# Kernel tuning notes

Measured on AMD Instinct MI355X. Metric: run time of the kernel, lower is better.

## Reference

```python
import jax, jax.numpy as jnp
import numpy as np

H = 16  # n_heads


def _ln(x, g, b, eps=1e-5):
    m = x.mean(-1, keepdims=True)
    v = ((x - m) ** 2).mean(-1, keepdims=True)
    return (x - m) / jnp.sqrt(v + eps) * g + b


def setup_inputs() -> dict:
    key = jax.random.key(0)
    ks = jax.random.split(key, 10)
    b, lq, d, dff, L = 2, 1024, 1024, 4096, 4
    s = 0.02
    return {
        "x": jax.random.normal(ks[0], (b, lq, d), jnp.float32),
        "memory_bank": jax.random.normal(ks[1], (L, b, lq, d), jnp.float32),
        "attn_mask": jax.random.bernoulli(ks[2], 0.3, (b, lq, lq)),
        "ln1_g": jnp.ones((d,), jnp.float32),
        "ln1_b": jnp.zeros((d,), jnp.float32),
        "Wq": jax.random.normal(ks[3], (d, d), jnp.float32) * s,
        "Wk": jax.random.normal(ks[4], (d, d), jnp.float32) * s,
        "Wv": jax.random.normal(ks[5], (d, d), jnp.float32) * s,
        "Wo": jax.random.normal(ks[6], (d, d), jnp.float32) * s,
        "ln2_g": jnp.ones((d,), jnp.float32),
        "ln2_b": jnp.zeros((d,), jnp.float32),
        "W1": jax.random.normal(ks[7], (d, dff), jnp.float32) * s,
        "b1": jnp.zeros((dff,), jnp.float32),
        "W2": jax.random.normal(ks[8], (dff, d), jnp.float32) * s,
        "b2": jnp.zeros((d,), jnp.float32),
    }


def reference(x, memory_bank, attn_mask, ln1_g, ln1_b, Wq, Wk, Wv, Wo,
              ln2_g, ln2_b, W1, b1, W2, b2):
    # x: [b, lq, d]; memory_bank: [L, b, lk, d]; attn_mask: [b, lq, lk] bool (True = masked)
    b, lq, d = x.shape
    dh = d // H
    # preprocess_attn: LayerNorm (eval mode -> dropouts are identity)
    q = _ln(x, ln1_g, ln1_b)
    # grow memory bank with current normalized input
    mem = jnp.concatenate([memory_bank, q[None]], axis=0)  # [L+1, b, lk, d]
    L, _, lk, _ = mem.shape
    # projections (bias-free); key/value projected per layer then flattened over (L, lk)
    pq = (q @ Wq).reshape(b, lq, H, dh).transpose(0, 2, 1, 3) * (dh ** -0.5)  # [b,h,lq,dh]
    pk = (mem @ Wk).transpose(1, 0, 2, 3).reshape(b, L * lk, H, dh).transpose(0, 2, 1, 3)
    pv = (mem @ Wv).transpose(1, 0, 2, 3).reshape(b, L * lk, H, dh).transpose(0, 2, 1, 3)
    scores = jnp.einsum('bhqd,bhkd->bhqk', pq, pk)           # [b,h,lq,L*lk]
    scores = scores.reshape(b, H, lq, L, lk)
    scores = jnp.where(attn_mask[:, None, :, None, :], -jnp.inf, scores)
    attn = jax.nn.softmax(scores.reshape(b, H, lq, L * lk), axis=-1)
    ctx = jnp.einsum('bhqk,bhkd->bhqd', attn, pv)            # [b,h,lq,dh]
    ctx = ctx.transpose(0, 2, 1, 3).reshape(b, lq, d)
    attn_out = ctx @ Wo
    # postprocess_attn: residual add
    x2 = x + attn_out
    # FFN: LayerNorm -> Linear -> ReLU -> Linear -> residual
    f = _ln(x2, ln2_g, ln2_b)
    f = jax.nn.relu(f @ W1 + b1) @ W2 + b2
    out = x2 + f
    return (out, mem)
```

## Files before the change

### kernel.cpp

```cpp
#include <hip/hip_runtime.h>
#include <hip/hip_bf16.h>

typedef __attribute__((ext_vector_type(8))) __bf16 bf16x8;
typedef __attribute__((ext_vector_type(4))) __bf16 bf16x4;
typedef __attribute__((ext_vector_type(4))) float f32x4;
typedef __attribute__((ext_vector_type(16))) float f32x16;

#define MFMA16(a, b, c) __builtin_amdgcn_mfma_f32_16x16x32_bf16((a), (b), (c), 0, 0, 0)
#define MFMA32(a, b, c) __builtin_amdgcn_mfma_f32_32x32x16_bf16((a), (b), (c), 0, 0, 0)
#define LOG2E 1.4426950408889634f

static __device__ __forceinline__ float exp2_fast(float x) {
    float r; asm("v_exp_f32 %0, %1" : "=v"(r) : "v"(x)); return r;
}

__device__ __forceinline__ void gll16(const void* g, void* l) {
    __builtin_amdgcn_global_load_lds((const __attribute__((address_space(1))) void*)g,
                                     (__attribute__((address_space(3))) void*)l,
                                     16, 0, 0);
}

__global__ __launch_bounds__(256) void prep_kernel(const float* __restrict__ bank,
                                                   float* __restrict__ mem_out,
                                                   __bf16* __restrict__ membf,
                                                   const float* __restrict__ x,
                                                   const float* __restrict__ g,
                                                   const float* __restrict__ bta,
                                                   float* __restrict__ q_out,
                                                   __bf16* __restrict__ qbf,
                                                   const float* __restrict__ Wq,
                                                   const float* __restrict__ Wk,
                                                   const float* __restrict__ Wv,
                                                   __bf16* __restrict__ Wq_t,
                                                   __bf16* __restrict__ Wkv_t) {
    __shared__ float rs[4], rs2[4];
    __shared__ float tile[32][33];
    int blk = blockIdx.x;
    if (blk < 2048) {
        int i = blk * 256 + threadIdx.x;
        const float4* i4 = (const float4*)bank;
        float4* o4 = (float4*)mem_out;
        for (; i < 2097152; i += 2048 * 256) {
            float4 v = i4[i];
            o4[i] = v;
            if (membf) {
                bf16x4 ob = {(__bf16)v.x, (__bf16)v.y, (__bf16)v.z, (__bf16)v.w};
                ((bf16x4*)membf)[i] = ob;
            }
        }
    } else if (blk < 4096) {
        int row = blk - 2048;
        const float4 v = ((const float4*)(x + (size_t)row * 1024))[threadIdx.x];
        float s = v.x + v.y + v.z + v.w;
        float s2 = v.x * v.x + v.y * v.y + v.z * v.z + v.w * v.w;
#pragma unroll
        for (int off = 1; off < 64; off <<= 1) {
            s += __shfl_xor(s, off);
            s2 += __shfl_xor(s2, off);
        }
        int wv = threadIdx.x >> 6;
        if ((threadIdx.x & 63) == 0) { rs[wv] = s; rs2[wv] = s2; }
        __syncthreads();
        s = rs[0] + rs[1] + rs[2] + rs[3];
        s2 = rs2[0] + rs2[1] + rs2[2] + rs2[3];
        float mean = s * (1.0f / 1024.0f);
        float var = s2 * (1.0f / 1024.0f) - mean * mean;
        float rstd = rsqrtf(var + 1e-5f);
        float4 gg = ((const float4*)g)[threadIdx.x];
        float4 bb = ((const float4*)bta)[threadIdx.x];
        float4 o;
        o.x = (v.x - mean) * rstd * gg.x + bb.x;
        o.y = (v.y - mean) * rstd * gg.y + bb.y;
        o.z = (v.z - mean) * rstd * gg.z + bb.z;
        o.w = (v.w - mean) * rstd * gg.w + bb.w;
        ((float4*)(q_out + (size_t)row * 1024))[threadIdx.x] = o;
        if (qbf) {
            bf16x4 ob = {(__bf16)o.x, (__bf16)o.y, (__bf16)o.z, (__bf16)o.w};
            ((bf16x4*)(qbf + (size_t)row * 1024))[threadIdx.x] = ob;
        }
    } else {
        int w = blk - 4096;
        int sel = w >> 10, within = w & 1023;
        const float* in = (sel == 0) ? Wq : ((sel == 1) ? Wk : Wv);
        __bf16* out = (sel == 0) ? Wq_t : (Wkv_t + (size_t)(sel - 1) * 1048576);
        int k0 = (within >> 5) * 32, n0 = (within & 31) * 32;
        int tx = threadIdx.x & 31, ty = threadIdx.x >> 5;
#pragma unroll
        for (int i = 0; i < 4; i++)
            tile[ty + i * 8][tx] = in[(size_t)(k0 + ty + i * 8) * 1024 + n0 + tx];
        __syncthreads();
#pragma unroll
        for (int i = 0; i < 4; i++)
            out[(size_t)(n0 + ty + i * 8) * 1024 + k0 + tx] = (__bf16)tile[tx][ty + i * 8];
    }
}

__global__ __launch_bounds__(256) void vtr_kernel(const __bf16* __restrict__ PV,
                                                  __bf16* __restrict__ PVt,
                                                  const unsigned char* __restrict__ mask,
                                                  unsigned int* __restrict__ mbits) {
    __shared__ __bf16 tile[64][72];
    int w = blockIdx.x;
    if (w < 2560) {
        int bh = w / 80, kt = w % 80;
        int b = bh >> 4, h = bh & 15;
        int lidx = kt >> 4, i0 = (kt & 15) * 64;
        int kg0 = lidx * 2048 + b * 1024 + i0;
        int r = threadIdx.x >> 2, c16 = (threadIdx.x & 3) * 16;
        const __bf16* src = PV + (size_t)(kg0 + r) * 1024 + h * 64 + c16;
        *(bf16x8*)&tile[r][c16] = *(const bf16x8*)src;
        *(bf16x8*)&tile[r][c16 + 8] = *(const bf16x8*)(src + 8);
        __syncthreads();
        int dh = threadIdx.x >> 2, k0 = (threadIdx.x & 3) * 16;
        bf16x8 o0, o1;
#pragma unroll
        for (int j = 0; j < 8; j++) {
            o0[j] = tile[k0 + j][dh];
            o1[j] = tile[k0 + 8 + j][dh];
        }
        __bf16* dst = PVt + (size_t)(bh * 64 + dh) * 5120 + kt * 64 + k0;
        *(bf16x8*)dst = o0;
        *(bf16x8*)(dst + 8) = o1;
    } else {
        int row = w - 2560;
        const unsigned char* mrow = mask + (size_t)row * 1024;
        int wv = threadIdx.x >> 6, l = threadIdx.x & 63;
        unsigned long long* dst = (unsigned long long*)(mbits + (size_t)row * 32);
#pragma unroll
        for (int i = 0; i < 4; i++) {
            int key = i * 256 + wv * 64 + l;
            unsigned long long bal = __ballot(mrow[key] != 0);
            if (l == 0) dst[i * 4 + wv] = bal;
        }
    }
}

__global__ __launch_bounds__(256) void ln_kernel(const float* __restrict__ x,
                                                 const float* __restrict__ g,
                                                 const float* __restrict__ bta,
                                                 __bf16* __restrict__ outb) {
    int row = blockIdx.x;
    const float4 v = ((const float4*)(x + (size_t)row * 1024))[threadIdx.x];
    float s = v.x + v.y + v.z + v.w;
    float s2 = v.x * v.x + v.y * v.y + v.z * v.z + v.w * v.w;
#pragma unroll
    for (int off = 1; off < 64; off <<= 1) {
        s += __shfl_xor(s, off);
        s2 += __shfl_xor(s2, off);
    }
    __shared__ float rs[4], rs2[4];
    int wv = threadIdx.x >> 6;
    if ((threadIdx.x & 63) == 0) { rs[wv] = s; rs2[wv] = s2; }
    __syncthreads();
    s = rs[0] + rs[1] + rs[2] + rs[3];
    s2 = rs2[0] + rs2[1] + rs2[2] + rs2[3];
    float mean = s * (1.0f / 1024.0f);
    float var = s2 * (1.0f / 1024.0f) - mean * mean;
    float rstd = rsqrtf(var + 1e-5f);
    float4 gg = ((const float4*)g)[threadIdx.x];
    float4 bb = ((const float4*)bta)[threadIdx.x];
    bf16x4 ob;
    ob[0] = (__bf16)((v.x - mean) * rstd * gg.x + bb.x);
    ob[1] = (__bf16)((v.y - mean) * rstd * gg.y + bb.y);
    ob[2] = (__bf16)((v.z - mean) * rstd * gg.z + bb.z);
    ob[3] = (__bf16)((v.w - mean) * rstd * gg.w + bb.w);
    ((bf16x4*)(outb + (size_t)row * 1024))[threadIdx.x] = ob;
}

__global__ __launch_bounds__(256) void comb_ln2(const float* __restrict__ pc0,
                                                const float* __restrict__ pc1,
                                                const float* __restrict__ x,
                                                const float* __restrict__ g,
                                                const float* __restrict__ bta,
                                                float* __restrict__ x2,
                                                __bf16* __restrict__ fln) {
    int row = blockIdx.x;
    int idx = row * 256 + threadIdx.x;
    float4 a = ((const float4*)pc0)[idx];
    float4 b = ((const float4*)pc1)[idx];
    float4 r = ((const float4*)x)[idx];
    float4 v;
    v.x = a.x + b.x + r.x;
    v.y = a.y + b.y + r.y;
    v.z = a.z + b.z + r.z;
    v.w = a.w + b.w + r.w;
    ((float4*)x2)[idx] = v;
    float s = v.x + v.y + v.z + v.w;
    float s2 = v.x * v.x + v.y * v.y + v.z * v.z + v.w * v.w;
#pragma unroll
    for (int off = 1; off < 64; off <<= 1) {
        s += __shfl_xor(s, off);
        s2 += __shfl_xor(s2, off);
    }
    __shared__ float rs[4], rs2[4];
    int wv = threadIdx.x >> 6;
    if ((threadIdx.x & 63) == 0) { rs[wv] = s; rs2[wv] = s2; }
    __syncthreads();
    s = rs[0] + rs[1] + rs[2] + rs[3];
    s2 = rs2[0] + rs2[1] + rs2[2] + rs2[3];
    float mean = s * (1.0f / 1024.0f);
    float var = s2 * (1.0f / 1024.0f) - mean * mean;
    float rstd = rsqrtf(var + 1e-5f);
    float4 gg = ((const float4*)g)[threadIdx.x];
    float4 bb = ((const float4*)bta)[threadIdx.x];
    bf16x4 ob;
    ob[0] = (__bf16)((v.x - mean) * rstd * gg.x + bb.x);
    ob[1] = (__bf16)((v.y - mean) * rstd * gg.y + bb.y);
    ob[2] = (__bf16)((v.z - mean) * rstd * gg.z + bb.z);
    ob[3] = (__bf16)((v.w - mean) * rstd * gg.w + bb.w);
    ((bf16x4*)(fln + (size_t)row * 1024))[threadIdx.x] = ob;
}

__device__ __forceinline__ void tr_body(const float* __restrict__ in, __bf16* __restrict__ out,
                                        int K, int N, int k0, int n0) {
    __shared__ float tile[32][33];
    int tx = threadIdx.x & 31, ty = threadIdx.x >> 5;
#pragma unroll
    for (int i = 0; i < 4; i++)
        tile[ty + i * 8][tx] = in[(size_t)(k0 + ty + i * 8) * N + n0 + tx];
    __syncthreads();
#pragma unroll
    for (int i = 0; i < 4; i++)
        out[(size_t)(n0 + ty + i * 8) * K + k0 + tx] = (__bf16)tile[tx][ty + i * 8];
}

__global__ __launch_bounds__(256) void tr_late(const float* __restrict__ Wo,
                                               const float* __restrict__ W1,
                                               const float* __restrict__ W2,
                                               __bf16* __restrict__ Wo_t,
                                               __bf16* __restrict__ W1_t,
                                               __bf16* __restrict__ W2_t) {
    int w = blockIdx.x;
    const float* in;
    __bf16* out;
    int K, N, k0, n0;
    if (w < 1024) {
        in = Wo; out = Wo_t; K = 1024; N = 1024; n0 = (w & 31) * 32; k0 = (w >> 5) * 32;
    } else if (w < 5120) {
        int v = w - 1024;
        in = W1; out = W1_t; K = 1024; N = 4096; n0 = (v & 127) * 32; k0 = (v >> 7) * 32;
    } else {
        int v = w - 5120;
        in = W2; out = W2_t; K = 4096; N = 1024; n0 = (v & 31) * 32; k0 = (v >> 5) * 32;
    }
    tr_body(in, out, K, N, k0, n0);
}

template <int EPI, bool ABF16>
__device__ __forceinline__ void gemm_core(const void* __restrict__ Av,
                                          const __bf16* __restrict__ Bt,
                                          void* __restrict__ Cout,
                                          const float* __restrict__ bias,
                                          const float* __restrict__ res,
                                          int N, int lda, int ldb, int klen,
                                          float scale, int bm, int bn) {
    constexpr int LDA = ABF16 ? 32 : 40;
    __shared__ __bf16 As[128 * LDA];
    __shared__ __bf16 Bs[128 * 32];

    int t = threadIdx.x;
    int lane = t & 63, wave = t >> 6;
    int wm = (wave >> 1) * 64, wn = (wave & 1) * 64;
    int l16 = lane & 15, l4 = lane >> 4;

    f32x4 acc[4][4];
#pragma unroll
    for (int m = 0; m < 4; m++)
#pragma unroll
        for (int n = 0; n < 4; n++) acc[m][n] = (f32x4){0.f, 0.f, 0.f, 0.f};

    int srow = t >> 2;
    int scol = (t & 3) * 8;
    int ar = t >> 1, ak = (t & 1) * 16;
    const __bf16* Ab = (const __bf16*)Av;
    const float* Af = (const float*)Av;

    for (int k0 = 0; k0 < klen; k0 += 32) {
        gll16(Bt + (size_t)(bn + srow) * ldb + (k0 + scol), &Bs[wave * 512]);
        gll16(Bt + (size_t)(bn + 64 + srow) * ldb + (k0 + scol), &Bs[2048 + wave * 512]);
        if constexpr (ABF16) {
            gll16(Ab + (size_t)(bm + srow) * lda + (k0 + scol), &As[wave * 512]);
            gll16(Ab + (size_t)(bm + 64 + srow) * lda + (k0 + scol), &As[2048 + wave * 512]);
        } else {
            const float* ap = Af + (size_t)(bm + ar) * lda + k0 + ak;
            float4 f0 = ((const float4*)ap)[0];
            float4 f1 = ((const float4*)ap)[1];
            float4 f2 = ((const float4*)ap)[2];
            float4 f3 = ((const float4*)ap)[3];
            float ta[16] = {f0.x, f0.y, f0.z, f0.w, f1.x, f1.y, f1.z, f1.w,
                            f2.x, f2.y, f2.z, f2.w, f3.x, f3.y, f3.z, f3.w};
            bf16x8 v0, v1;
#pragma unroll
            for (int j = 0; j < 8; j++) { v0[j] = (__bf16)ta[j]; v1[j] = (__bf16)ta[j + 8]; }
            *(bf16x8*)&As[ar * 40 + ak] = v0;
            *(bf16x8*)&As[ar * 40 + ak + 8] = v1;
        }
        __syncthreads();

        bf16x8 af[4], bfr[4];
#pragma unroll
        for (int m = 0; m < 4; m++) af[m] = *(const bf16x8*)&As[(wm + m * 16 + l16) * LDA + l4 * 8];
#pragma unroll
        for (int n = 0; n < 4; n++) bfr[n] = *(const bf16x8*)&Bs[(wn + n * 16 + l16) * 32 + l4 * 8];
#pragma unroll
        for (int m = 0; m < 4; m++)
#pragma unroll
            for (int n = 0; n < 4; n++) acc[m][n] = MFMA16(af[m], bfr[n], acc[m][n]);
        __syncthreads();
    }

#pragma unroll
    for (int m = 0; m < 4; m++) {
#pragma unroll
        for (int r = 0; r < 4; r++) {
            int row = bm + wm + m * 16 + l4 * 4 + r;
#pragma unroll
            for (int n = 0; n < 4; n++) {
                int col = bn + wn + n * 16 + l16;
                float c = acc[m][n][r];
                size_t idx = (size_t)row * N + col;
                if (EPI == 0) {
                    ((__bf16*)Cout)[idx] = (__bf16)(c * scale);
                } else if (EPI == 1) {
                    ((float*)Cout)[idx] = c + res[idx];
                } else if (EPI == 2) {
                    ((__bf16*)Cout)[idx] = (__bf16)fmaxf(c + bias[col], 0.0f);
                } else if (EPI == 3) {
                    ((float*)Cout)[idx] = c + bias[col] + res[idx];
                } else {
                    ((float*)Cout)[idx] = c;
                }
            }
        }
    }
}

template <int EPI, bool ABF16>
__global__ __launch_bounds__(256) void gemm_bt(const void* __restrict__ Av,
                                               const __bf16* __restrict__ Bt,
                                               void* __restrict__ Cout,
                                               const float* __restrict__ bias,
                                               const float* __restrict__ res,
                                               int N, int K, float scale, int nbx) {
    int q = gridDim.x >> 3;
    int swz = (blockIdx.x & 7) * q + (blockIdx.x >> 3);
    int bn = (swz % nbx) * 128;
    int bm = (swz / nbx) * 128;
    gemm_core<EPI, ABF16>(Av, Bt, Cout, bias, res, N, K, K, K, scale, bm, bn);
}

template <bool ABF16>
__global__ __launch_bounds__(256) void gemm_proj(const void* __restrict__ Akv,
                                                 const __bf16* __restrict__ Wkv_t,
                                                 __bf16* __restrict__ PK,
                                                 __bf16* __restrict__ PV,
                                                 const void* __restrict__ Aq,
                                                 const __bf16* __restrict__ Wq_t,
                                                 __bf16* __restrict__ Pq) {
    int q = gridDim.x >> 3;
    int swz = (blockIdx.x & 7) * q + (blockIdx.x >> 3);
    if (swz < 1280) {
        int bn = (swz & 15) * 128, bm = (swz >> 4) * 128;
        __bf16* C = (bn < 1024) ? PK : PV;
        int bnl = bn & 1023;
        const __bf16* Bt = Wkv_t + ((size_t)(bn & 1024) << 10);
        gemm_core<0, ABF16>(Akv, Bt, C, nullptr, nullptr, 1024, 1024, 1024, 1024, 1.0f, bm, bnl);
    } else {
        int p = swz - 1280;
        int bn = (p & 7) * 128, bm = (p >> 3) * 128;
        gemm_core<0, ABF16>(Aq, Wq_t, Pq, nullptr, nullptr, 1024, 1024, 1024, 1024,
                            0.125f * LOG2E, bm, bn);
    }
}

__global__ __launch_bounds__(256) void gemm_w2(const __bf16* __restrict__ h1,
                                               const __bf16* __restrict__ W2_t,
                                               float* __restrict__ pc0,
                                               float* __restrict__ pc1) {
    int q = gridDim.x >> 3;
    int swz = (blockIdx.x & 7) * q + (blockIdx.x >> 3);
    int half = swz >> 7;
    int p = swz & 127;
    int bn = (p & 7) * 128, bm = (p >> 3) * 128;
    int koff = half * 2048;
    gemm_core<4, true>(h1 + koff, W2_t + koff, half ? pc1 : pc0, nullptr, nullptr,
                       1024, 4096, 4096, 2048, 1.0f, bm, bn);
}

__global__ __launch_bounds__(256) void gemm_wo(const __bf16* __restrict__ ctx,
                                               const __bf16* __restrict__ Wo_t,
                                               float* __restrict__ pc0,
                                               float* __restrict__ pc1) {
    int q = gridDim.x >> 3;
    int swz = (blockIdx.x & 7) * q + (blockIdx.x >> 3);
    int half = swz >> 7;
    int p = swz & 127;
    int bn = (p & 7) * 128, bm = (p >> 3) * 128;
    int koff = half * 512;
    gemm_core<4, true>(ctx + koff, Wo_t + koff, half ? pc1 : pc0, nullptr, nullptr,
                       1024, 1024, 1024, 512, 1.0f, bm, bn);
}

__global__ __launch_bounds__(256) void comb_kernel(const float* __restrict__ pc0,
                                                   const float* __restrict__ pc1,
                                                   const float* __restrict__ bias,
                                                   const float* __restrict__ res,
                                                   float* __restrict__ out) {
    int i = blockIdx.x * 256 + threadIdx.x;
    float4 a = ((const float4*)pc0)[i];
    float4 b = ((const float4*)pc1)[i];
    float4 r = ((const float4*)res)[i];
    float4 o;
    o.x = a.x + b.x + r.x;
    o.y = a.y + b.y + r.y;
    o.z = a.z + b.z + r.z;
    o.w = a.w + b.w + r.w;
    if (bias) {
        float4 bb = ((const float4*)bias)[i & 255];
        o.x += bb.x; o.y += bb.y; o.z += bb.z; o.w += bb.w;
    }
    ((float4*)out)[i] = o;
}

__device__ __forceinline__ void softmax_p(const f32x16& s0, const f32x16& s1,
                                          unsigned int mka, unsigned int mkb,
                                          int hi, float& lsum, bf16x8* pf) {
    unsigned int ow[8][2];
#pragma unroll
    for (int g = 0; g < 4; g++) {
        bf16x4 p0, p1;
#pragma unroll
        for (int m = 0; m < 4; m++) {
            float e = exp2_fast(s0[g * 4 + m]);
            e = ((mka >> (g * 8 + hi * 4 + m)) & 1u) ? 0.0f : e;
            lsum += e;
            p0[m] = (__bf16)e;
            float e2 = exp2_fast(s1[g * 4 + m]);
            e2 = ((mkb >> (g * 8 + hi * 4 + m)) & 1u) ? 0.0f : e2;
            lsum += e2;
            p1[m] = (__bf16)e2;
        }
        ow[g][0] = ((unsigned int*)&p0)[0];
        ow[g][1] = ((unsigned int*)&p0)[1];
        ow[4 + g][0] = ((unsigned int*)&p1)[0];
        ow[4 + g][1] = ((unsigned int*)&p1)[1];
    }
#pragma unroll
    for (int ks = 0; ks < 4; ks++) {
        unsigned int a0 = ow[2 * ks][0], b0 = ow[2 * ks + 1][0];
        unsigned int a1 = ow[2 * ks][1], b1 = ow[2 * ks + 1][1];
        asm volatile("v_permlane32_swap_b32 %0, %1" : "+v"(a0), "+v"(b0));
        asm volatile("v_permlane32_swap_b32 %0, %1" : "+v"(a1), "+v"(b1));
        unsigned int* pp = (unsigned int*)&pf[ks];
        pp[0] = a0; pp[1] = a1; pp[2] = b0; pp[3] = b1;
    }
}

#define NCHP 20
__global__ __launch_bounds__(256, 2) void attn_part(const __bf16* __restrict__ Pq,
                                                    const __bf16* __restrict__ PK,
                                                    const __bf16* __restrict__ PVt,
                                                    const unsigned int* __restrict__ mbits,
                                                    __bf16* __restrict__ pacc,
                                                    float* __restrict__ pl) {
    int bh = blockIdx.x;
    int b = bh >> 4, h = bh & 15;
    int rng = blockIdx.z;
    int wave = threadIdx.x >> 6, lane = threadIdx.x & 63;
    int l32 = lane & 31, hi = lane >> 5;
    int q0 = blockIdx.y * 256 + wave * 64;

    __shared__ __bf16 KB[2][64][64];
    __shared__ __bf16 VB[2][64][64];

    bf16x8 qf[2][4];
#pragma unroll
    for (int tile = 0; tile < 2; tile++) {
        const __bf16* pqrow = Pq + (size_t)(b * 1024 + q0 + tile * 32 + l32) * 1024 + h * 64 + hi * 8;
#pragma unroll
        for (int ds = 0; ds < 4; ds++) qf[tile][ds] = *(const bf16x8*)(pqrow + ds * 16);
    }

    f32x16 acc00, acc01, acc10, acc11;
#pragma unroll
    for (int i = 0; i < 16; i++) { acc00[i] = 0.f; acc01[i] = 0.f; acc10[i] = 0.f; acc11[i] = 0.f; }
    float lsum0 = 0.0f, lsum1 = 0.0f;

    const unsigned int* mrow0 = mbits + (size_t)(b * 1024 + q0 + l32) * 32;
    const unsigned int* mrow1 = mbits + (size_t)(b * 1024 + q0 + 32 + l32) * 32;

    int kgbase = rng * 1280;

    int idxA = wave * 8 + (lane >> 3);
    int idxB = (wave + 4) * 8 + (lane >> 3);
    int GA = (idxA ^ (idxA >> 3)) & 7;
    int GB = (idxB ^ (idxB >> 3)) & 7;
    int swA = (((lane & 7) ^ GA) << 4);
    int swB = (((lane & 7) ^ GB) << 4);
    size_t koffA = (size_t)idxA * 2048 + swA;
    size_t koffB = (size_t)idxB * 2048 + swB;
    size_t voffA = (size_t)idxA * 10240 + swA;
    size_t voffB = (size_t)idxB * 10240 + swB;

    int kmod = kgbase & 1023;
    const char* pkc = (const char*)PK + ((size_t)((kgbase >> 10) * 2048 + b * 1024 + kmod)) * 2048
                      + (size_t)h * 128;
    const char* pvc = (const char*)PVt + (size_t)(bh * 64) * 10240 + (size_t)kgbase * 2;

#define STAGE(BUF)                                            \
    do {                                                      \
        gll16(pkc + koffA, &KB[BUF][wave * 8][0]);            \
        gll16(pkc + koffB, &KB[BUF][(wave + 4) * 8][0]);      \
        gll16(pvc + voffA, &VB[BUF][wave * 8][0]);            \
        gll16(pvc + voffB, &VB[BUF][(wave + 4) * 8][0]);      \
    } while (0)
#define ADV()                                                          \
    do {                                                               \
        int st = (kmod + 64 >= 1024) ? (64 + 1024) : 64;               \
        kmod = (kmod + 64) & 1023;                                     \
        pkc += (size_t)st * 2048;                                      \
        pvc += 128;                                                    \
    } while (0)

    STAGE(0);
    ADV();
    int kd0 = (kgbase & 1023) >> 5;
    unsigned int mk0a = mrow0[kd0], mk0b = mrow0[kd0 + 1];
    unsigned int mk1a = mrow1[kd0], mk1b = mrow1[kd0 + 1];

    int Gr0 = (l32 ^ (l32 >> 3)) & 7;
    int r1v = 32 + l32;
    int Gr1 = (r1v ^ (r1v >> 3)) & 7;

    for (int t = 0; t < NCHP; t++) {
        int buf = t & 1;
        __syncthreads();
        if (t + 1 < NCHP) {
            STAGE(buf ^ 1);
            ADV();
        }
        unsigned int nk0a = 0, nk0b = 0, nk1a = 0, nk1b = 0;
        if (t + 1 < NCHP) {
            int kdn = ((kgbase + (t + 1) * 64) & 1023) >> 5;
            nk0a = mrow0[kdn]; nk0b = mrow0[kdn + 1];
            nk1a = mrow1[kdn]; nk1b = mrow1[kdn + 1];
        }

        const __bf16* KsF = &KB[buf][0][0];
        const __bf16* VtF = &VB[buf][0][0];

        f32x16 s00, s01, s10, s11;
#pragma unroll
        for (int i = 0; i < 16; i++) { s00[i] = 0.f; s01[i] = 0.f; s10[i] = 0.f; s11[i] = 0.f; }
        __builtin_amdgcn_s_setprio(1);
#pragma unroll
        for (int ds = 0; ds < 4; ds++) {
            bf16x8 ka0 = *(const bf16x8*)&KsF[l32 * 64 + (((ds * 2 + hi) ^ Gr0) << 3)];
            bf16x8 ka1 = *(const bf16x8*)&KsF[r1v * 64 + (((ds * 2 + hi) ^ Gr1) << 3)];
            s00 = MFMA32(ka0, qf[0][ds], s00);
            s10 = MFMA32(ka0, qf[1][ds], s10);
            s01 = MFMA32(ka1, qf[0][ds], s01);
            s11 = MFMA32(ka1, qf[1][ds], s11);
        }
        __builtin_amdgcn_s_setprio(0);

        bf16x8 pf0[4], pf1[4];
        softmax_p(s00, s01, mk0a, mk0b, hi, lsum0, pf0);
        softmax_p(s10, s11, mk1a, mk1b, hi, lsum1, pf1);

        mk0a = nk0a; mk0b = nk0b; mk1a = nk1a; mk1b = nk1b;

        __builtin_amdgcn_s_setprio(1);
#pragma unroll
        for (int ks = 0; ks < 4; ks++) {
            bf16x8 vf0 = *(const bf16x8*)&VtF[l32 * 64 + (((ks * 2 + hi) ^ Gr0) << 3)];
            bf16x8 vf1 = *(const bf16x8*)&VtF[r1v * 64 + (((ks * 2 + hi) ^ Gr1) << 3)];
            acc00 = MFMA32(vf0, pf0[ks], acc00);
            acc01 = MFMA32(vf1, pf0[ks], acc01);
            acc10 = MFMA32(vf0, pf1[ks], acc10);
            acc11 = MFMA32(vf1, pf1[ks], acc11);
        }
        __builtin_amdgcn_s_setprio(0);
    }
#undef STAGE
#undef ADV

    lsum0 += __shfl_xor(lsum0, 32);
    lsum1 += __shfl_xor(lsum1, 32);

    size_t blk = ((size_t)(bh * 4 + blockIdx.y) * 4 + rng);
    __bf16* pa0 = pacc + blk * 16384 + (size_t)(wave * 64 + l32) * 64;
    __bf16* pa1 = pacc + blk * 16384 + (size_t)(wave * 64 + 32 + l32) * 64;
#pragma unroll
    for (int g = 0; g < 4; g++) {
        bf16x4 o00, o01, o10, o11;
#pragma unroll
        for (int m = 0; m < 4; m++) {
            o00[m] = (__bf16)acc00[g * 4 + m];
            o01[m] = (__bf16)acc01[g * 4 + m];
            o10[m] = (__bf16)acc10[g * 4 + m];
            o11[m] = (__bf16)acc11[g * 4 + m];
        }
        *(bf16x4*)&pa0[g * 8 + hi * 4] = o00;
        *(bf16x4*)&pa0[32 + g * 8 + hi * 4] = o01;
        *(bf16x4*)&pa1[g * 8 + hi * 4] = o10;
        *(bf16x4*)&pa1[32 + g * 8 + hi * 4] = o11;
    }
    if (hi == 0) {
        pl[blk * 256 + wave * 64 + l32] = lsum0;
        pl[blk * 256 + wave * 64 + 32 + l32] = lsum1;
    }
}

__global__ __launch_bounds__(512) void attn_comb(const __bf16* __restrict__ pacc,
                                                 const float* __restrict__ pl,
                                                 __bf16* __restrict__ ctx) {
    int bh = blockIdx.x, qb = blockIdx.y;
    int b = bh >> 4, h = bh & 15;
    int q = threadIdx.x >> 1, dhalf = (threadIdx.x & 1) * 32;
    float acc[32];
#pragma unroll
    for (int j = 0; j < 32; j++) acc[j] = 0.0f;
    float l = 0.0f;
    size_t blk0 = ((size_t)(bh * 4 + qb)) * 4;
#pragma unroll
    for (int rng = 0; rng < 4; rng++) {
        size_t base = (blk0 + rng) * 16384 + (size_t)q * 64 + dhalf;
#pragma unroll
        for (int v = 0; v < 4; v++) {
            bf16x8 a = *(const bf16x8*)&pacc[base + v * 8];
#pragma unroll
            for (int j = 0; j < 8; j++) acc[v * 8 + j] += (float)a[j];
        }
        l += pl[(blk0 + rng) * 256 + q];
    }
    float inv = 1.0f / l;
    __bf16* crow = ctx + ((size_t)(b * 1024 + qb * 256 + q) << 10) + h * 64 + dhalf;
#pragma unroll
    for (int v = 0; v < 4; v++) {
        bf16x8 o;
#pragma unroll
        for (int j = 0; j < 8; j++) o[j] = (__bf16)(acc[v * 8 + j] * inv);
        *(bf16x8*)&crow[v * 8] = o;
    }
}

#define KHALF 2560
#define CK 64
#define NCH 40
__global__ __launch_bounds__(512, 4) void attn_kernel(const __bf16* __restrict__ Pq,
                                                      const __bf16* __restrict__ PK,
                                                      const __bf16* __restrict__ PV,
                                                      const unsigned char* __restrict__ mask,
                                                      __bf16* __restrict__ ctx) {
    int bh = blockIdx.x;
    int b = bh >> 4, h = bh & 15;
    int wave = threadIdx.x >> 6, lane = threadIdx.x & 63;
    int grp = wave >> 2, wv = wave & 3;
    int l16 = lane & 15, l4 = lane >> 4;
    int q0 = blockIdx.y * 64 + wv * 16;

    __shared__ __bf16 Ks[2][64][72];
    __shared__ __bf16 Vt[2][64][72];
    __shared__ __bf16 Ps[8][16][72];

    const f32x4 fzero = {0.f, 0.f, 0.f, 0.f};

    bf16x8 qf[2];
    {
        const __bf16* pqrow = Pq + (size_t)(b * 1024 + q0 + l16) * 1024 + h * 64;
        qf[0] = *(const bf16x8*)(pqrow + l4 * 8);
        qf[1] = *(const bf16x8*)(pqrow + 32 + l4 * 8);
    }

    f32x4 accT[4];
#pragma unroll
    for (int n = 0; n < 4; n++) accT[n] = fzero;
    float lsum = 0.0f;

    const unsigned char* mrow_p = mask + (size_t)b * (1024u * 1024u) + (size_t)(q0 + l16) * 1024;

    int tl = threadIdx.x & 255;
    int skey = tl >> 2;
    int sd0 = (tl & 3) << 4;
    int kgbase = grp * KHALF;

    bf16x8 rk0, rk1, rv0, rv1;
    unsigned int mk[4], mkn[4];
    {
        int kg = kgbase + skey;
        int lidx = kg >> 10, i = kg & 1023;
        size_t off = (size_t)(lidx * 2048 + b * 1024 + i) * 1024 + h * 64 + sd0;
        rk0 = *(const bf16x8*)(PK + off);
        rk1 = *(const bf16x8*)(PK + off + 8);
        rv0 = *(const bf16x8*)(PV + off);
        rv1 = *(const bf16x8*)(PV + off + 8);
        int kloc = kgbase & 1023;
#pragma unroll
        for (int tile = 0; tile < 4; tile++)
            mk[tile] = *(const unsigned int*)(mrow_p + kloc + tile * 16 + l4 * 4);
    }

    for (int t = 0; t < NCH; t++) {
        *(bf16x8*)&Ks[grp][skey][sd0] = rk0;
        *(bf16x8*)&Ks[grp][skey][sd0 + 8] = rk1;
#pragma unroll
        for (int j = 0; j < 8; j++) {
            int row = sd0 + j;
            Vt[grp][row][skey ^ ((row >> 3) << 3)] = rv0[j];
            int row2 = sd0 + 8 + j;
            Vt[grp][row2][skey ^ ((row2 >> 3) << 3)] = rv1[j];
        }
        __syncthreads();

        if (t + 1 < NCH) {
            int kg = kgbase + (t + 1) * CK + skey;
            int lidx = kg >> 10, i = kg & 1023;
            size_t off = (size_t)(lidx * 2048 + b * 1024 + i) * 1024 + h * 64 + sd0;
            rk0 = *(const bf16x8*)(PK + off);
            rk1 = *(const bf16x8*)(PK + off + 8);
            rv0 = *(const bf16x8*)(PV + off);
            rv1 = *(const bf16x8*)(PV + off + 8);
            int kloc = (kgbase + (t + 1) * CK) & 1023;
#pragma unroll
            for (int tile = 0; tile < 4; tile++)
                mkn[tile] = *(const unsigned int*)(mrow_p + kloc + tile * 16 + l4 * 4);
        }

        f32x4 s[4];
        __builtin_amdgcn_s_setprio(1);
#pragma unroll
        for (int tile = 0; tile < 4; tile++) {
            bf16x8 ka = *(const bf16x8*)&Ks[grp][tile * 16 + l16][l4 * 8];
            bf16x8 kb = *(const bf16x8*)&Ks[grp][tile * 16 + l16][32 + l4 * 8];
            f32x4 sz = fzero;
            sz = MFMA16(ka, qf[0], sz);
            sz = MFMA16(kb, qf[1], sz);
            s[tile] = sz;
        }
        __builtin_amdgcn_s_setprio(0);

        float psum = 0.0f;
#pragma unroll
        for (int tile = 0; tile < 4; tile++) {
            bf16x4 pk_;
#pragma unroll
            for (int r = 0; r < 4; r++) {
                float e = exp2_fast(s[tile][r]);
                e = ((mk[tile] >> (r * 8)) & 255u) ? 0.0f : e;
                psum += e;
                pk_[r] = (__bf16)e;
            }
            *(bf16x4*)&Ps[wave][l16][tile * 16 + l4 * 4] = pk_;
        }
        lsum += psum;
#pragma unroll
        for (int tile = 0; tile < 4; tile++) mk[tile] = mkn[tile];

        __builtin_amdgcn_s_setprio(1);
#pragma unroll
        for (int kk = 0; kk < 2; kk++) {
            bf16x8 pf = *(const bf16x8*)&Ps[wave][l16][kk * 32 + l4 * 8];
#pragma unroll
            for (int n = 0; n < 4; n++) {
                int row = n * 16 + l16;
                int colblk = (kk * 32 + l4 * 8) ^ ((row >> 3) << 3);
                bf16x8 vf = *(const bf16x8*)&Vt[grp][row][colblk];
                accT[n] = MFMA16(vf, pf, accT[n]);
            }
        }
        __builtin_amdgcn_s_setprio(0);
        __syncthreads();
    }

    lsum += __shfl_xor(lsum, 16);
    lsum += __shfl_xor(lsum, 32);

    float* exAcc = (float*)&Ks[0][0][0];
    float* exL = (float*)&Vt[0][0][0];
    if (grp == 1) {
#pragma unroll
        for (int n = 0; n < 4; n++)
            *(f32x4*)&exAcc[(wv * 16 + l16) * 68 + n * 16 + l4 * 4] = accT[n];
        if (l4 == 0) exL[wv * 16 + l16] = lsum;
    }
    __syncthreads();
    if (grp == 0) {
        int qi = wv * 16 + l16;
        float inv = 1.0f / (lsum + exL[qi]);
        __bf16* crow = ctx + ((size_t)(b * 1024 + q0 + l16) << 10) + h * 64;
#pragma unroll
        for (int n = 0; n < 4; n++) {
            f32x4 a1 = *(const f32x4*)&exAcc[qi * 68 + n * 16 + l4 * 4];
            bf16x4 o;
#pragma unroll
            for (int r = 0; r < 4; r++) o[r] = (__bf16)((accT[n][r] + a1[r]) * inv);
            *(bf16x4*)&crow[n * 16 + l4 * 4] = o;
        }
    }
}

extern "C" void kernel_launch(void* const* d_in, const int* in_sizes, int n_in,
                              void* d_out, int out_size, void* d_ws, size_t ws_size,
                              hipStream_t stream) {
    const float* x = (const float*)d_in[0];
    const float* memory_bank = (const float*)d_in[1];
    const unsigned char* attn_mask = (const unsigned char*)d_in[2];
    const float* ln1_g = (const float*)d_in[3];
    const float* ln1_b = (const float*)d_in[4];
    const float* Wq = (const float*)d_in[5];
    const float* Wk = (const float*)d_in[6];
    const float* Wv = (const float*)d_in[7];
    const float* Wo = (const float*)d_in[8];
    const float* ln2_g = (const float*)d_in[9];
    const float* ln2_b = (const float*)d_in[10];
    const float* W1 = (const float*)d_in[11];
    const float* b1 = (const float*)d_in[12];
    const float* W2 = (const float*)d_in[13];
    const float* b2 = (const float*)d_in[14];

    float* out = (float*)d_out;
    float* mem_out = out + 2097152;
    float* q_out = mem_out + 4 * 2097152;

    char* ws = (char*)d_ws;
    bool big = ws_size >= (70ull << 20);

    __bf16* PK = (__bf16*)ws;
    __bf16* PV = (__bf16*)(ws + (20ull << 20));
    __bf16 *Pq, *Wq_t, *Wkv_t, *ctx, *membf = nullptr, *qbf = nullptr;
    __bf16* PVt = nullptr;
    __bf16* pacc = nullptr;
    float* plv = nullptr;
    unsigned int* mbits = nullptr;
    if (big) {
        membf = (__bf16*)(ws + (40ull << 20));
        qbf = membf + (size_t)8192 * 1024;
        Wq_t = (__bf16*)(ws + (60ull << 20));
        Wkv_t = (__bf16*)(ws + (62ull << 20));
        Pq = (__bf16*)(ws + (66ull << 20));
        PVt = (__bf16*)(ws + (40ull << 20));
        mbits = (unsigned int*)(ws + (60ull << 20));
        pacc = (__bf16*)(ws + (20ull << 20));
        plv = (float*)(ws + (36ull << 20));
        ctx = (__bf16*)(ws + (60ull << 20));
    } else {
        Pq = (__bf16*)(ws + (40ull << 20));
        Wq_t = (__bf16*)(ws + (44ull << 20));
        Wkv_t = (__bf16*)(ws + (46ull << 20));
        ctx = (__bf16*)(ws + (44ull << 20));
    }
    __bf16* Wo_t = (__bf16*)ws;
    __bf16* W1_t = (__bf16*)(ws + (2ull << 20));
    __bf16* W2_t = (__bf16*)(ws + (10ull << 20));
    float* x2 = (float*)(ws + (18ull << 20));
    __bf16* fln = (__bf16*)(ws + (26ull << 20));
    __bf16* h1 = (__bf16*)(ws + (30ull << 20));
    float* wo_pc0 = (float*)(ws + (30ull << 20));
    float* wo_pc1 = (float*)(ws + (38ull << 20));
    float* pc0 = (float*)(ws + (46ull << 20));
    float* pc1 = (float*)(ws + (54ull << 20));

    prep_kernel<<<7168, 256, 0, stream>>>(memory_bank, mem_out, membf, x, ln1_g, ln1_b,
                                          q_out, qbf, Wq, Wk, Wv, Wq_t, Wkv_t);

    if (big)
        gemm_proj<true><<<1408, 256, 0, stream>>>(membf, Wkv_t, PK, PV, qbf, Wq_t, Pq);
    else
        gemm_proj<false><<<1408, 256, 0, stream>>>(mem_out, Wkv_t, PK, PV, q_out, Wq_t, Pq);

    if (big) {
        vtr_kernel<<<4608, 256, 0, stream>>>(PV, PVt, attn_mask, mbits);
        attn_part<<<dim3(32, 4, 4), 256, 0, stream>>>(Pq, PK, PVt, mbits, pacc, plv);
        attn_comb<<<dim3(32, 4), 512, 0, stream>>>(pacc, plv, ctx);
    } else {
        attn_kernel<<<dim3(32, 16), 512, 0, stream>>>(Pq, PK, PV, attn_mask, ctx);
    }

    tr_late<<<9216, 256, 0, stream>>>(Wo, W1, W2, Wo_t, W1_t, W2_t);

    if (big) {
        gemm_wo<<<256, 256, 0, stream>>>(ctx, Wo_t, wo_pc0, wo_pc1);
        comb_ln2<<<2048, 256, 0, stream>>>(wo_pc0, wo_pc1, x, ln2_g, ln2_b, x2, fln);
    } else {
        gemm_bt<1, true><<<128, 256, 0, stream>>>(ctx, Wo_t, x2, nullptr, x, 1024, 1024, 1.0f, 8);
        ln_kernel<<<2048, 256, 0, stream>>>(x2, ln2_g, ln2_b, fln);
    }
    gemm_bt<2, true><<<512, 256, 0, stream>>>(fln, W1_t, h1, b1, nullptr, 4096, 1024, 1.0f, 32);
    if (big) {
        gemm_w2<<<256, 256, 0, stream>>>(h1, W2_t, pc0, pc1);
        comb_kernel<<<2048, 256, 0, stream>>>(pc0, pc1, b2, x2, out);
    } else {
        gemm_bt<3, true><<<128, 256, 0, stream>>>(h1, W2_t, out, b2, x2, 1024, 4096, 1.0f, 8);
    }
}
```

Measured before the change: 272.9 us.

## Add K=64 bf16 GEMM core with direct-to-LDS loads and 8-way attention split

Adds a new bf16 GEMM core that stages 128x64 A/B tiles via global_load_lds with an XOR swizzle and runs 16x16x32 MFMAs. It is used for the QKV projection, Wo, W1 and W2 GEMMs on the large-workspace path. The attention partial kernel is templated on the number of key ranges, and 8 ranges are used when the workspace is at least 104 MB, giving more blocks for occupancy. The cost is more partial output for the combine step. The new GEMM core is single-buffered with two barriers per K step, so load latency may not be hidden as well as in the old core.

```diff
diff --git a/kernel.cpp b/kernel.cpp
--- a/kernel.cpp
+++ b/kernel.cpp
@@ -335,6 +335,100 @@
     }
 }
 
+template <int EPI>
+__device__ __forceinline__ void gemm_core64(const __bf16* __restrict__ Ab,
+                                            const __bf16* __restrict__ Bt,
+                                            void* __restrict__ Cout,
+                                            const float* __restrict__ bias,
+                                            const float* __restrict__ res,
+                                            int N, int lda, int ldb, int klen,
+                                            float scale, int bm, int bn) {
+    __shared__ __bf16 As[128 * 64];
+    __shared__ __bf16 Bs[128 * 64];
+
+    int t = threadIdx.x;
+    int lane = t & 63, wave = t >> 6;
+    int wm = (wave >> 1) * 64, wn = (wave & 1) * 64;
+    int l16 = lane & 15, l4 = lane >> 4;
+
+    f32x4 acc[4][4];
+#pragma unroll
+    for (int m = 0; m < 4; m++)
+#pragma unroll
+        for (int n = 0; n < 4; n++) acc[m][n] = (f32x4){0.f, 0.f, 0.f, 0.f};
+
+    int lrow = lane >> 3, lg = lane & 7;
+    size_t srcA[4], srcB[4];
+    __bf16 *dstA[4], *dstB[4];
+#pragma unroll
+    for (int c = 0; c < 4; c++) {
+        int grow = c * 32 + wave * 8 + lrow;
+        int G = (grow ^ (grow >> 3)) & 7;
+        srcA[c] = (size_t)(bm + grow) * lda + ((lg ^ G) << 3);
+        srcB[c] = (size_t)(bn + grow) * ldb + ((lg ^ G) << 3);
+        dstA[c] = &As[(c * 32 + wave * 8) * 64];
+        dstB[c] = &Bs[(c * 32 + wave * 8) * 64];
+    }
+    int GA[4], GB[4];
+#pragma unroll
+    for (int m = 0; m < 4; m++) {
+        int ra = wm + m * 16 + l16;
+        GA[m] = (ra ^ (ra >> 3)) & 7;
+        int rb = wn + m * 16 + l16;
+        GB[m] = (rb ^ (rb >> 3)) & 7;
+    }
+
+    for (int k0 = 0; k0 < klen; k0 += 64) {
+#pragma unroll
+        for (int c = 0; c < 4; c++) {
+            gll16(Ab + srcA[c] + k0, dstA[c]);
+            gll16(Bt + srcB[c] + k0, dstB[c]);
+        }
+        __syncthreads();
+#pragma unroll
+        for (int kh = 0; kh < 2; kh++) {
+            bf16x8 af[4], bfr[4];
+#pragma unroll
+            for (int m = 0; m < 4; m++) {
+                int ga = (kh * 4 + l4) ^ GA[m];
+                af[m] = *(const bf16x8*)&As[(wm + m * 16 + l16) * 64 + ga * 8];
+                int gb = (kh * 4 + l4) ^ GB[m];
+                bfr[m] = *(const bf16x8*)&Bs[(wn + m * 16 + l16) * 64 + gb * 8];
+            }
+#pragma unroll
+            for (int m = 0; m < 4; m++)
+#pragma unroll
+                for (int n = 0; n < 4; n++) acc[m][n] = MFMA16(af[m], bfr[n], acc[m][n]);
+        }
+        __syncthreads();
+    }
+
+#pragma unroll
+    for (int m = 0; m < 4; m++) {
+#pragma unroll
+        for (int r = 0; r < 4; r++) {
+            int row = bm + wm + m * 16 + l4 * 4 + r;
+#pragma unroll
+            for (int n = 0; n < 4; n++) {
+                int col = bn + wn + n * 16 + l16;
+                float c = acc[m][n][r];
+                size_t idx = (size_t)row * N + col;
+                if (EPI == 0) {
+                    ((__bf16*)Cout)[idx] = (__bf16)(c * scale);
+                } else if (EPI == 1) {
+                    ((float*)Cout)[idx] = c + res[idx];
+                } else if (EPI == 2) {
+                    ((__bf16*)Cout)[idx] = (__bf16)fmaxf(c + bias[col], 0.0f);
+                } else if (EPI == 3) {
+                    ((float*)Cout)[idx] = c + bias[col] + res[idx];
+                } else {
+                    ((float*)Cout)[idx] = c;
+                }
+            }
+        }
+    }
+}
+
 template <int EPI, bool ABF16>
 __global__ __launch_bounds__(256) void gemm_bt(const void* __restrict__ Av,
                                                const __bf16* __restrict__ Bt,
@@ -349,14 +443,27 @@
     gemm_core<EPI, ABF16>(Av, Bt, Cout, bias, res, N, K, K, K, scale, bm, bn);
 }
 
-template <bool ABF16>
-__global__ __launch_bounds__(256) void gemm_proj(const void* __restrict__ Akv,
-                                                 const __bf16* __restrict__ Wkv_t,
-                                                 __bf16* __restrict__ PK,
-                                                 __bf16* __restrict__ PV,
-                                                 const void* __restrict__ Aq,
-                                                 const __bf16* __restrict__ Wq_t,
-                                                 __bf16* __restrict__ Pq) {
+template <int EPI>
+__global__ __launch_bounds__(256) void gemm_bt64(const __bf16* __restrict__ Ab,
+                                                 const __bf16* __restrict__ Bt,
+                                                 void* __restrict__ Cout,
+                                                 const float* __restrict__ bias,
+                                                 const float* __restrict__ res,
+                                                 int N, int K, float scale, int nbx) {
+    int q = gridDim.x >> 3;
+    int swz = (blockIdx.x & 7) * q + (blockIdx.x >> 3);
+    int bn = (swz % nbx) * 128;
+    int bm = (swz / nbx) * 128;
+    gemm_core64<EPI>(Ab, Bt, Cout, bias, res, N, K, K, K, scale, bm, bn);
+}
+
+__global__ __launch_bounds__(256) void gemm_proj64(const __bf16* __restrict__ Akv,
+                                                   const __bf16* __restrict__ Wkv_t,
+                                                   __bf16* __restrict__ PK,
+                                                   __bf16* __restrict__ PV,
+                                                   const __bf16* __restrict__ Aq,
+                                                   const __bf16* __restrict__ Wq_t,
+                                                   __bf16* __restrict__ Pq) {
     int q = gridDim.x >> 3;
     int swz = (blockIdx.x & 7) * q + (blockIdx.x >> 3);
     if (swz < 1280) {
@@ -364,11 +471,34 @@
         __bf16* C = (bn < 1024) ? PK : PV;
         int bnl = bn & 1023;
         const __bf16* Bt = Wkv_t + ((size_t)(bn & 1024) << 10);
-        gemm_core<0, ABF16>(Akv, Bt, C, nullptr, nullptr, 1024, 1024, 1024, 1024, 1.0f, bm, bnl);
+        gemm_core64<0>(Akv, Bt, C, nullptr, nullptr, 1024, 1024, 1024, 1024, 1.0f, bm, bnl);
     } else {
         int p = swz - 1280;
         int bn = (p & 7) * 128, bm = (p >> 3) * 128;
-        gemm_core<0, ABF16>(Aq, Wq_t, Pq, nullptr, nullptr, 1024, 1024, 1024, 1024,
+        gemm_core64<0>(Aq, Wq_t, Pq, nullptr, nullptr, 1024, 1024, 1024, 1024,
+                       0.125f * LOG2E, bm, bn);
+    }
+}
+
+__global__ __launch_bounds__(256) void gemm_proj_f32(const void* __restrict__ Akv,
+                                                     const __bf16* __restrict__ Wkv_t,
+                                                     __bf16* __restrict__ PK,
+                                                     __bf16* __restrict__ PV,
+                                                     const void* __restrict__ Aq,
+                                                     const __bf16* __restrict__ Wq_t,
+                                                     __bf16* __restrict__ Pq) {
+    int q = gridDim.x >> 3;
+    int swz = (blockIdx.x & 7) * q + (blockIdx.x >> 3);
+    if (swz < 1280) {
+        int bn = (swz & 15) * 128, bm = (swz >> 4) * 128;
+        __bf16* C = (bn < 1024) ? PK : PV;
+        int bnl = bn & 1023;
+        const __bf16* Bt = Wkv_t + ((size_t)(bn & 1024) << 10);
+        gemm_core<0, false>(Akv, Bt, C, nullptr, nullptr, 1024, 1024, 1024, 1024, 1.0f, bm, bnl);
+    } else {
+        int p = swz - 1280;
+        int bn = (p & 7) * 128, bm = (p >> 3) * 128;
+        gemm_core<0, false>(Aq, Wq_t, Pq, nullptr, nullptr, 1024, 1024, 1024, 1024,
                             0.125f * LOG2E, bm, bn);
     }
 }
@@ -383,8 +513,8 @@
     int p = swz & 127;
     int bn = (p & 7) * 128, bm = (p >> 3) * 128;
     int koff = half * 2048;
-    gemm_core<4, true>(h1 + koff, W2_t + koff, half ? pc1 : pc0, nullptr, nullptr,
-                       1024, 4096, 4096, 2048, 1.0f, bm, bn);
+    gemm_core64<4>(h1 + koff, W2_t + koff, half ? pc1 : pc0, nullptr, nullptr,
+                   1024, 4096, 4096, 2048, 1.0f, bm, bn);
 }
 
 __global__ __launch_bounds__(256) void gemm_wo(const __bf16* __restrict__ ctx,
@@ -397,8 +527,8 @@
     int p = swz & 127;
     int bn = (p & 7) * 128, bm = (p >> 3) * 128;
     int koff = half * 512;
-    gemm_core<4, true>(ctx + koff, Wo_t + koff, half ? pc1 : pc0, nullptr, nullptr,
-                       1024, 1024, 1024, 512, 1.0f, bm, bn);
+    gemm_core64<4>(ctx + koff, Wo_t + koff, half ? pc1 : pc0, nullptr, nullptr,
+                   1024, 1024, 1024, 512, 1.0f, bm, bn);
 }
 
 __global__ __launch_bounds__(256) void comb_kernel(const float* __restrict__ pc0,
@@ -456,13 +586,14 @@
     }
 }
 
-#define NCHP 20
+template <int NRNG>
 __global__ __launch_bounds__(256, 2) void attn_part(const __bf16* __restrict__ Pq,
                                                     const __bf16* __restrict__ PK,
                                                     const __bf16* __restrict__ PVt,
                                                     const unsigned int* __restrict__ mbits,
                                                     __bf16* __restrict__ pacc,
                                                     float* __restrict__ pl) {
+    constexpr int NCHP_ = 5120 / NRNG / 64;
     int bh = blockIdx.x;
     int b = bh >> 4, h = bh & 15;
     int rng = blockIdx.z;
@@ -489,14 +620,14 @@
     const unsigned int* mrow0 = mbits + (size_t)(b * 1024 + q0 + l32) * 32;
     const unsigned int* mrow1 = mbits + (size_t)(b * 1024 + q0 + 32 + l32) * 32;
 
-    int kgbase = rng * 1280;
+    int kgbase = rng * (5120 / NRNG);
 
     int idxA = wave * 8 + (lane >> 3);
     int idxB = (wave + 4) * 8 + (lane >> 3);
-    int GA = (idxA ^ (idxA >> 3)) & 7;
-    int GB = (idxB ^ (idxB >> 3)) & 7;
-    int swA = (((lane & 7) ^ GA) << 4);
-    int swB = (((lane & 7) ^ GB) << 4);
+    int GAi = (idxA ^ (idxA >> 3)) & 7;
+    int GBi = (idxB ^ (idxB >> 3)) & 7;
+    int swA = (((lane & 7) ^ GAi) << 4);
+    int swB = (((lane & 7) ^ GBi) << 4);
     size_t koffA = (size_t)idxA * 2048 + swA;
     size_t koffB = (size_t)idxB * 2048 + swB;
     size_t voffA = (size_t)idxA * 10240 + swA;
@@ -532,15 +663,15 @@
     int r1v = 32 + l32;
     int Gr1 = (r1v ^ (r1v >> 3)) & 7;
 
-    for (int t = 0; t < NCHP; t++) {
+    for (int t = 0; t < NCHP_; t++) {
         int buf = t & 1;
         __syncthreads();
-        if (t + 1 < NCHP) {
+        if (t + 1 < NCHP_) {
             STAGE(buf ^ 1);
             ADV();
         }
         unsigned int nk0a = 0, nk0b = 0, nk1a = 0, nk1b = 0;
-        if (t + 1 < NCHP) {
+        if (t + 1 < NCHP_) {
             int kdn = ((kgbase + (t + 1) * 64) & 1023) >> 5;
             nk0a = mrow0[kdn]; nk0b = mrow0[kdn + 1];
             nk1a = mrow1[kdn]; nk1b = mrow1[kdn + 1];
@@ -588,7 +719,7 @@
     lsum0 += __shfl_xor(lsum0, 32);
     lsum1 += __shfl_xor(lsum1, 32);
 
-    size_t blk = ((size_t)(bh * 4 + blockIdx.y) * 4 + rng);
+    size_t blk = ((size_t)(bh * 4 + blockIdx.y) * NRNG + rng);
     __bf16* pa0 = pacc + blk * 16384 + (size_t)(wave * 64 + l32) * 64;
     __bf16* pa1 = pacc + blk * 16384 + (size_t)(wave * 64 + 32 + l32) * 64;
 #pragma unroll
@@ -612,6 +743,7 @@
     }
 }
 
+template <int NRNG>
 __global__ __launch_bounds__(512) void attn_comb(const __bf16* __restrict__ pacc,
                                                  const float* __restrict__ pl,
                                                  __bf16* __restrict__ ctx) {
@@ -622,9 +754,9 @@
 #pragma unroll
     for (int j = 0; j < 32; j++) acc[j] = 0.0f;
     float l = 0.0f;
-    size_t blk0 = ((size_t)(bh * 4 + qb)) * 4;
-#pragma unroll
-    for (int rng = 0; rng < 4; rng++) {
+    size_t blk0 = ((size_t)(bh * 4 + qb)) * NRNG;
+#pragma unroll
+    for (int rng = 0; rng < NRNG; rng++) {
         size_t base = (blk0 + rng) * 16384 + (size_t)q * 64 + dhalf;
 #pragma unroll
         for (int v = 0; v < 4; v++) {
@@ -825,6 +957,7 @@
 
     char* ws = (char*)d_ws;
     bool big = ws_size >= (70ull << 20);
+    bool r8 = big && ws_size >= (104ull << 20);
 
     __bf16* PK = (__bf16*)ws;
     __bf16* PV = (__bf16*)(ws + (20ull << 20));
@@ -841,8 +974,13 @@
         Pq = (__bf16*)(ws + (66ull << 20));
         PVt = (__bf16*)(ws + (40ull << 20));
         mbits = (unsigned int*)(ws + (60ull << 20));
-        pacc = (__bf16*)(ws + (20ull << 20));
-        plv = (float*)(ws + (36ull << 20));
+        if (r8) {
+            pacc = (__bf16*)(ws + (70ull << 20));
+            plv = (float*)(ws + (102ull << 20));
+        } else {
+            pacc = (__bf16*)(ws + (20ull << 20));
+            plv = (float*)(ws + (36ull << 20));
+        }
         ctx = (__bf16*)(ws + (60ull << 20));
     } else {
         Pq = (__bf16*)(ws + (40ull << 20));
@@ -865,14 +1003,19 @@
                                           q_out, qbf, Wq, Wk, Wv, Wq_t, Wkv_t);
 
     if (big)
-        gemm_proj<true><<<1408, 256, 0, stream>>>(membf, Wkv_t, PK, PV, qbf, Wq_t, Pq);
+        gemm_proj64<<<1408, 256, 0, stream>>>(membf, Wkv_t, PK, PV, qbf, Wq_t, Pq);
     else
-        gemm_proj<false><<<1408, 256, 0, stream>>>(mem_out, Wkv_t, PK, PV, q_out, Wq_t, Pq);
+        gemm_proj_f32<<<1408, 256, 0, stream>>>(mem_out, Wkv_t, PK, PV, q_out, Wq_t, Pq);
 
     if (big) {
         vtr_kernel<<<4608, 256, 0, stream>>>(PV, PVt, attn_mask, mbits);
-        attn_part<<<dim3(32, 4, 4), 256, 0, stream>>>(Pq, PK, PVt, mbits, pacc, plv);
-        attn_comb<<<dim3(32, 4), 512, 0, stream>>>(pacc, plv, ctx);
+        if (r8) {
+            attn_part<8><<<dim3(32, 4, 8), 256, 0, stream>>>(Pq, PK, PVt, mbits, pacc, plv);
+            attn_comb<8><<<dim3(32, 4), 512, 0, stream>>>(pacc, plv, ctx);
+        } else {
+            attn_part<4><<<dim3(32, 4, 4), 256, 0, stream>>>(Pq, PK, PVt, mbits, pacc, plv);
+            attn_comb<4><<<dim3(32, 4), 512, 0, stream>>>(pacc, plv, ctx);
+        }
     } else {
         attn_kernel<<<dim3(32, 16), 512, 0, stream>>>(Pq, PK, PV, attn_mask, ctx);
     }
@@ -886,7 +1029,10 @@
         gemm_bt<1, true><<<128, 256, 0, stream>>>(ctx, Wo_t, x2, nullptr, x, 1024, 1024, 1.0f, 8);
         ln_kernel<<<2048, 256, 0, stream>>>(x2, ln2_g, ln2_b, fln);
     }
-    gemm_bt<2, true><<<512, 256, 0, stream>>>(fln, W1_t, h1, b1, nullptr, 4096, 1024, 1.0f, 32);
+    if (big)
+        gemm_bt64<2><<<512, 256, 0, stream>>>(fln, W1_t, h1, b1, nullptr, 4096, 1024, 1.0f, 32);
+    else
+        gemm_bt<2, true><<<512, 256, 0, stream>>>(fln, W1_t, h1, b1, nullptr, 4096, 1024, 1.0f, 32);
     if (big) {
         gemm_w2<<<256, 256, 0, stream>>>(h1, W2_t, pc0, pc1);
         comb_kernel<<<2048, 256, 0, stream>>>(pc0, pc1, b2, x2, out);
```

Measured after the change: 292.9 us. 7.3% more time.
